# Optimization experiments

Measured on AMD Instinct MI355X. Metric: run time of the kernel, lower is better.

## Reference

```python
import jax, jax.numpy as jnp
import numpy as np

N_NODES = 50000
N_EDGES = 600000
D_IN = 128
D = 128
N_REL = 2
N_LAYERS = 3


def rgcn_conv(h, src, dst, edge_type, weight, root, bias):
    # PyG RGCNConv (no bases), aggr='mean' per relation:
    # out_i = h_i @ root + bias + sum_r mean_{j in N_r(i)} h_j @ W_r
    out = h @ root + bias                      # [N, D]
    hs = h[src]                                # [E, D] gather once
    for r in range(N_REL):
        mask = (edge_type == r).astype(h.dtype)          # [E]
        agg = jax.ops.segment_sum(hs * mask[:, None], dst, num_segments=N_NODES)  # [N, D]
        cnt = jax.ops.segment_sum(mask, dst, num_segments=N_NODES)                # [N]
        mean = agg / jnp.maximum(cnt, 1.0)[:, None]
        out = out + mean @ weight[r]
    return out


def setup_inputs() -> dict:
    key = jax.random.key(0)
    ks = jax.random.split(key, 10)
    x = jax.random.normal(ks[0], (N_NODES, D_IN), dtype=jnp.float32)
    edge_index = jax.random.randint(ks[1], (2, N_EDGES), 0, N_NODES, dtype=jnp.int64)
    edge_attr = jax.random.normal(ks[2], (N_EDGES, N_REL), dtype=jnp.float32)
    # input projection f: Linear(D_IN, D); stored as [D_IN, D] (apply as x @ Wf + bf)
    Wf = jax.random.normal(ks[3], (D_IN, D), dtype=jnp.float32) / np.sqrt(D_IN)
    bf = jnp.zeros((D,), dtype=jnp.float32)
    # per-layer RGCNConv params, stacked over layers
    conv_weight = jax.random.normal(ks[4], (N_LAYERS, N_REL, D, D), dtype=jnp.float32) / np.sqrt(D)
    conv_root = jax.random.normal(ks[5], (N_LAYERS, D, D), dtype=jnp.float32) / np.sqrt(D)
    conv_bias = jnp.zeros((N_LAYERS, D), dtype=jnp.float32)
    return {"x": x, "edge_index": edge_index, "edge_attr": edge_attr,
            "Wf": Wf, "bf": bf, "conv_weight": conv_weight,
            "conv_root": conv_root, "conv_bias": conv_bias}


def reference(x, edge_index, edge_attr, Wf, bf, conv_weight, conv_root, conv_bias):
    src, dst = edge_index[0], edge_index[1]
    edge_type = jnp.argmax(edge_attr, axis=1)           # [E]
    h = jax.nn.relu(x @ Wf + bf)                        # [N, D]
    for l in range(N_LAYERS):
        h = rgcn_conv(h, src, dst, edge_type, conv_weight[l], conv_root[l], conv_bias[l])
        h = jax.nn.relu(h)
    return h
```

## Files before the change

### kernel.cpp

```cpp
#include <hip/hip_runtime.h>
#include <hip/hip_bf16.h>

#define NN 50000
#define NE 600000
#define D 128
#define NREL 2
#define BM 128

typedef __attribute__((ext_vector_type(8))) short bf16x8;
typedef __attribute__((ext_vector_type(4))) float f32x4;
typedef __attribute__((ext_vector_type(2))) float f32x2;

__device__ __forceinline__ float bf2f(short s) {
    return __uint_as_float(((unsigned int)(unsigned short)s) << 16);
}
__device__ __forceinline__ bf16x8 pack_bf8(const float* a) {
    union { bf16x8 v; __hip_bfloat162 h2[4]; } o;
#pragma unroll
    for (int i = 0; i < 4; i++)
        o.h2[i] = __float22bfloat162_rn(make_float2(a[2 * i], a[2 * i + 1]));
    return o.v;
}

#define NEB ((NE + 255) / 256)
#define NWT (16384 + 3 * 49152)
#define NWB ((NWT + 255) / 256)

__global__ void k_pre1(const float* __restrict__ attr,
                       const int* __restrict__ dst,
                       int* __restrict__ cnt,
                       const float* __restrict__ Wf,
                       const float* __restrict__ cw,
                       const float* __restrict__ cr,
                       __hip_bfloat16* __restrict__ wt) {
    if (blockIdx.x < NEB) {
        int i = blockIdx.x * blockDim.x + threadIdx.x;
        if (i >= NE) return;
        float2 a = reinterpret_cast<const float2*>(attr)[i];
        int r = (a.y > a.x) ? 1 : 0;
        atomicAdd(&cnt[dst[i] * 2 + r], 1);
    } else {
        int idx = (blockIdx.x - NEB) * blockDim.x + threadIdx.x;
        if (idx >= NWT) return;
        float v;
        if (idx < 16384) {
            int n = idx >> 7, k = idx & 127;
            v = Wf[k * 128 + n];
        } else {
            int j = idx - 16384;
            int l = j / 49152; j %= 49152;
            int n = j / 384, k = j % 384;
            if (k < 128)      v = cr[((size_t)l * 128 + k) * 128 + n];
            else if (k < 256) v = cw[((size_t)(l * 2 + 0) * 128 + (k - 128)) * 128 + n];
            else              v = cw[((size_t)(l * 2 + 1) * 128 + (k - 256)) * 128 + n];
        }
        wt[idx] = __float2bfloat16(v);
    }
}

__global__ void k_pre2(const int* __restrict__ cnt, float* __restrict__ inv,
                       int* __restrict__ off, int* __restrict__ cur,
                       int* __restrict__ total) {
    int i = blockIdx.x * blockDim.x + threadIdx.x;
    if (i >= NN) return;
    int c0 = cnt[2 * i], c1 = cnt[2 * i + 1];
    inv[2 * i]     = 1.0f / (float)(c0 > 1 ? c0 : 1);
    inv[2 * i + 1] = 1.0f / (float)(c1 > 1 ? c1 : 1);
    int o = atomicAdd(total, c0 + c1);
    off[2 * i] = o;       cur[2 * i] = o;
    off[2 * i + 1] = o + c0; cur[2 * i + 1] = o + c0;
}

__global__ void k_fill(const float* __restrict__ attr,
                       const int* __restrict__ src, const int* __restrict__ dst,
                       int* __restrict__ cursor, int* __restrict__ srcs, int E) {
    int i = blockIdx.x * blockDim.x + threadIdx.x;
    if (i >= E) return;
    float2 a = reinterpret_cast<const float2*>(attr)[i];
    int r = (a.y > a.x) ? 1 : 0;
    int pos = atomicAdd(&cursor[dst[i] * 2 + r], 1);
    srcs[pos] = src[i];
}

__global__ __launch_bounds__(256)
void k_aggregate(const __hip_bfloat16* __restrict__ h,
                 const int* __restrict__ srcs,
                 const int* __restrict__ off, const int* __restrict__ cnt,
                 const float* __restrict__ inv,
                 __hip_bfloat16* __restrict__ agg) {
    int wid = (blockIdx.x * blockDim.x + threadIdx.x) >> 6;
    int lane = threadIdx.x & 63;
    int nb = wid * 4;
    if (nb >= NN) return;
    const int g = lane >> 4, l16 = lane & 15;
    int node = nb + g;
    bool nv = node < NN;
    int nn = nv ? node : (NN - 1);

    int st  = off[2 * nn];
    int c0  = nv ? cnt[2 * nn] : 0;
    int c01 = c0 + (nv ? cnt[2 * nn + 1] : 0);
    float i0 = inv[2 * nn], i1 = inv[2 * nn + 1];

    int sv = (l16 < c01) ? srcs[st + l16] : 0;

    int cm = c01;
    cm = max(cm, __shfl_xor(cm, 16));
    cm = max(cm, __shfl_xor(cm, 32));

    f32x2 a0[4], a1[4];
#pragma unroll
    for (int p = 0; p < 4; p++) { a0[p] = (f32x2)(0.f); a1[p] = (f32x2)(0.f); }

    const char* hb = (const char*)h;
    for (int j = 0; j < cm; j += 4) {
        int s[4]; float w0[4], w1[4];
#pragma unroll
        for (int q = 0; q < 4; ++q) {
            int jj = j + q;
            int t = __shfl(sv, (lane & 48) + (jj & 15));
            s[q] = t;
            if (jj >= 16 && jj < c01) s[q] = srcs[st + jj];
            if (jj >= c01) s[q] = 0;
            w0[q] = (jj < c0) ? i0 : 0.f;
            w1[q] = (jj >= c0 && jj < c01) ? i1 : 0.f;
        }
        uint4 v[4];
#pragma unroll
        for (int q = 0; q < 4; ++q)
            v[q] = *reinterpret_cast<const uint4*>(
                hb + (size_t)s[q] * 256 + l16 * 16);
#pragma unroll
        for (int q = 0; q < 4; ++q) {
            f32x2 w0v = {w0[q], w0[q]}, w1v = {w1[q], w1[q]};
            unsigned uu[4] = {v[q].x, v[q].y, v[q].z, v[q].w};
#pragma unroll
            for (int p = 0; p < 4; ++p) {
                f32x2 val;
                val.x = __uint_as_float(uu[p] << 16);
                val.y = __uint_as_float(uu[p] & 0xffff0000u);
                a0[p] += val * w0v;
                a1[p] += val * w1v;
            }
        }
    }

    if (!nv) return;
    float t0[8], t1[8];
#pragma unroll
    for (int p = 0; p < 4; p++) {
        t0[2 * p] = a0[p].x; t0[2 * p + 1] = a0[p].y;
        t1[2 * p] = a1[p].x; t1[2 * p + 1] = a1[p].y;
    }
    __hip_bfloat16* dp = agg + (size_t)node * 256;
    *reinterpret_cast<bf16x8*>(dp + l16 * 8)       = pack_bf8(t0);
    *reinterpret_cast<bf16x8*>(dp + 128 + l16 * 8) = pack_bf8(t1);
}

__global__ __launch_bounds__(256)
void k_gemm_proj(const float* __restrict__ X,
                 const __hip_bfloat16* __restrict__ Wt,
                 const float* __restrict__ bias,
                 __hip_bfloat16* __restrict__ out, int N) {
    __shared__ uint4 sB4[1024];
    char* sB = (char*)sB4;
    const int tid = threadIdx.x;
    const int w = tid >> 6;
    const int l16 = tid & 15, lg = (tid & 63) >> 4;

    f32x4 acc[2][8];
#pragma unroll
    for (int m = 0; m < 2; m++)
#pragma unroll
        for (int n = 0; n < 8; n++) acc[m][n] = (f32x4)(0.f);

    const int row0 = blockIdx.x * 128;
#pragma unroll
    for (int kb = 0; kb < 2; ++kb) {
        bf16x8 afr[2][2];
#pragma unroll
        for (int mb = 0; mb < 2; ++mb)
#pragma unroll
            for (int kk = 0; kk < 2; ++kk) {
                int r = row0 + w * 32 + mb * 16 + l16;
                if (r >= N) r = N - 1;
                const float* p = X + (size_t)r * D + kb * 64 + kk * 32 + lg * 8;
                float4 u0 = reinterpret_cast<const float4*>(p)[0];
                float4 u1 = reinterpret_cast<const float4*>(p)[1];
                float t[8] = {u0.x, u0.y, u0.z, u0.w, u1.x, u1.y, u1.z, u1.w};
                afr[mb][kk] = pack_bf8(t);
            }
        __syncthreads();
        {
            int trow = tid >> 3, tb = (tid & 7) * 16;
#pragma unroll
            for (int p = 0; p < 4; ++p) {
                int rr = trow + p * 32;
                uint4 v = *reinterpret_cast<const uint4*>(
                    (const char*)(Wt + (size_t)rr * 128 + kb * 64) + tb);
                *reinterpret_cast<uint4*>(sB + rr * 128 + (tb ^ ((rr & 7) << 4))) = v;
            }
        }
        __syncthreads();
#pragma unroll
        for (int kk = 0; kk < 2; ++kk)
#pragma unroll
            for (int nb = 0; nb < 8; ++nb) {
                int brow = nb * 16 + l16;
                int bcol = kk * 64 + lg * 16;
                bf16x8 bfr = *reinterpret_cast<const bf16x8*>(
                    sB + brow * 128 + (bcol ^ ((brow & 7) << 4)));
                acc[0][nb] = __builtin_amdgcn_mfma_f32_16x16x32_bf16(
                    afr[0][kk], bfr, acc[0][nb], 0, 0, 0);
                acc[1][nb] = __builtin_amdgcn_mfma_f32_16x16x32_bf16(
                    afr[1][kk], bfr, acc[1][nb], 0, 0, 0);
            }
    }
#pragma unroll
    for (int nb = 0; nb < 8; ++nb) {
        int n = nb * 16 + l16;
        float bv = bias[n];
#pragma unroll
        for (int mb = 0; mb < 2; ++mb)
#pragma unroll
            for (int r = 0; r < 4; ++r) {
                int grow = row0 + w * 32 + mb * 16 + lg * 4 + r;
                if (grow < N) {
                    float v = acc[mb][nb][r] + bv;
                    v = v > 0.f ? v : 0.f;
                    out[(size_t)grow * D + n] = __float2bfloat16(v);
                }
            }
    }
}

template <bool OUT_F32>
__global__ __launch_bounds__(256)
void k_gemm_mfma(const __hip_bfloat16* __restrict__ A0, int sA0,
                 const __hip_bfloat16* __restrict__ A1, int sA1,
                 const __hip_bfloat16* __restrict__ A2, int sA2,
                 const __hip_bfloat16* __restrict__ Wt,
                 const float* __restrict__ bias,
                 void* __restrict__ outv, int N) {
    __shared__ uint4 sB4[1024];
    char* sB = (char*)sB4;
    const int tid = threadIdx.x;
    const int w = tid >> 6;
    const int l16 = tid & 15, lg = (tid & 63) >> 4;
    const __hip_bfloat16* As[3] = {A0, A1, A2};
    const int strides[3] = {sA0, sA1, sA2};

    f32x4 acc[2][8];
#pragma unroll
    for (int m = 0; m < 2; m++)
#pragma unroll
        for (int n = 0; n < 8; n++) acc[m][n] = (f32x4)(0.f);

    const size_t row0 = (size_t)blockIdx.x * BM;
#pragma unroll
    for (int kb = 0; kb < 6; ++kb) {
        const __hip_bfloat16* Ac = As[kb >> 1];
        const int strideC = strides[kb >> 1];
        const int koff = (kb & 1) * 64;
        bf16x8 afr[2][2];
#pragma unroll
        for (int mb = 0; mb < 2; ++mb)
#pragma unroll
            for (int kk = 0; kk < 2; ++kk) {
                int r = (int)row0 + w * 32 + mb * 16 + l16;
                if (r >= N) r = N - 1;
                afr[mb][kk] = *reinterpret_cast<const bf16x8*>(
                    Ac + (size_t)r * strideC + koff + kk * 32 + lg * 8);
            }
        __syncthreads();
        {
            int trow = tid >> 3;
            int tb = (tid & 7) * 16;
#pragma unroll
            for (int p = 0; p < 4; ++p) {
                int rr = trow + p * 32;
                uint4 v = *reinterpret_cast<const uint4*>(
                    (const char*)(Wt + (size_t)rr * 384 + kb * 64) + tb);
                *reinterpret_cast<uint4*>(sB + rr * 128 + (tb ^ ((rr & 7) << 4))) = v;
            }
        }
        __syncthreads();
#pragma unroll
        for (int kk = 0; kk < 2; ++kk) {
#pragma unroll
            for (int nb = 0; nb < 8; ++nb) {
                int brow = nb * 16 + l16;
                int bcol = kk * 64 + lg * 16;
                bf16x8 bfr = *reinterpret_cast<const bf16x8*>(
                    sB + brow * 128 + (bcol ^ ((brow & 7) << 4)));
                acc[0][nb] = __builtin_amdgcn_mfma_f32_16x16x32_bf16(
                    afr[0][kk], bfr, acc[0][nb], 0, 0, 0);
                acc[1][nb] = __builtin_amdgcn_mfma_f32_16x16x32_bf16(
                    afr[1][kk], bfr, acc[1][nb], 0, 0, 0);
            }
        }
    }
#pragma unroll
    for (int nb = 0; nb < 8; ++nb) {
        int n = nb * 16 + l16;
        float bv = bias[n];
#pragma unroll
        for (int mb = 0; mb < 2; ++mb) {
#pragma unroll
            for (int r = 0; r < 4; ++r) {
                long grow = (long)row0 + w * 32 + mb * 16 + lg * 4 + r;
                if (grow < N) {
                    float v = acc[mb][nb][r] + bv;
                    v = v > 0.f ? v : 0.f;
                    if (OUT_F32)
                        ((float*)outv)[(size_t)grow * D + n] = v;
                    else
                        ((__hip_bfloat16*)outv)[(size_t)grow * D + n] =
                            __float2bfloat16(v);
                }
            }
        }
    }
}

extern "C" void kernel_launch(void* const* d_in, const int* in_sizes, int n_in,
                              void* d_out, int out_size, void* d_ws, size_t ws_size,
                              hipStream_t stream) {
    const float* x    = (const float*)d_in[0];
    const int*   ei   = (const int*)d_in[1];
    const float* attr = (const float*)d_in[2];
    const float* Wf   = (const float*)d_in[3];
    const float* bf   = (const float*)d_in[4];
    const float* cw   = (const float*)d_in[5];
    const float* cr   = (const float*)d_in[6];
    const float* cb   = (const float*)d_in[7];
    const int* src  = ei;
    const int* dstv = ei + NE;

    char* p = (char*)d_ws;
    __hip_bfloat16* h0   = (__hip_bfloat16*)p; p += (size_t)NN * D * 2;
    __hip_bfloat16* h1   = (__hip_bfloat16*)p; p += (size_t)NN * D * 2;
    __hip_bfloat16* aggb = (__hip_bfloat16*)p; p += (size_t)2 * NN * D * 2;
    __hip_bfloat16* wt   = (__hip_bfloat16*)p; p += (size_t)NWT * 2;
    float* inv  = (float*)p;                p += (size_t)2 * NN * 4;
    int*   cnt  = (int*)p;                  p += (size_t)2 * NN * 4;
    int*   off  = (int*)p;                  p += (size_t)2 * NN * 4;
    int*   cur  = (int*)p;                  p += (size_t)2 * NN * 4;
    int*   srcs = (int*)p;                  p += (size_t)NE * 4;
    int*   total= (int*)p;

    float* outp = (float*)d_out;

    hipMemsetAsync(cnt, 0, (size_t)2 * NN * sizeof(int), stream);
    hipMemsetAsync(total, 0, sizeof(int), stream);
    k_pre1<<<NEB + NWB, 256, 0, stream>>>(attr, dstv, cnt, Wf, cw, cr, wt);
    k_pre2<<<(NN + 255) / 256, 256, 0, stream>>>(cnt, inv, off, cur, total);
    k_fill<<<NEB, 256, 0, stream>>>(attr, src, dstv, cur, srcs, NE);

    k_gemm_proj<<<(NN + 127) / 128, 256, 0, stream>>>(x, wt, bf, h0, NN);

    const int gblocks = (NN + BM - 1) / BM;
    const int ablocks = ((NN + 3) / 4 * 64 + 255) / 256;
    for (int l = 0; l < 3; ++l) {
        const __hip_bfloat16* hin = (l == 1) ? h1 : h0;
        k_aggregate<<<ablocks, 256, 0, stream>>>(hin, srcs, off, cnt, inv, aggb);
        const __hip_bfloat16* wl = wt + 16384 + (size_t)l * 49152;
        const float* bl = cb + (size_t)l * D;
        if (l == 2) {
            k_gemm_mfma<true><<<gblocks, 256, 0, stream>>>(
                hin, 128, aggb, 256, aggb + 128, 256, wl, bl, outp, NN);
        } else {
            __hip_bfloat16* hout = (l == 0) ? h1 : h0;
            k_gemm_mfma<false><<<gblocks, 256, 0, stream>>>(
                hin, 128, aggb, 256, aggb + 128, 256, wl, bl, hout, NN);
        }
    }
}
```

Baseline: 230.2 us.

## Sort nodes by degree so aggregate wavefronts process similar-degree nodes

Adds a degree histogram, a single-block scan and a scatter pass that build a permutation of nodes ordered by descending total in-degree. The aggregate kernel then gives each wavefront four nodes of similar degree, which cuts divergence from the per-wave max-degree loop bound. It also adds a fast path for waves whose max degree fits in the 16 preloaded source indices. The cost is three extra small preprocessing launches with atomics, and output rows are now written in scattered rather than sequential order.

```diff
diff --git a/kernel.cpp b/kernel.cpp
--- a/kernel.cpp
+++ b/kernel.cpp
@@ -6,6 +6,7 @@
 #define D 128
 #define NREL 2
 #define BM 128
+#define NBIN 512
 
 typedef __attribute__((ext_vector_type(8))) short bf16x8;
 typedef __attribute__((ext_vector_type(4))) float f32x4;
@@ -60,7 +61,7 @@
 
 __global__ void k_pre2(const int* __restrict__ cnt, float* __restrict__ inv,
                        int* __restrict__ off, int* __restrict__ cur,
-                       int* __restrict__ total) {
+                       int* __restrict__ total, int* __restrict__ hist) {
     int i = blockIdx.x * blockDim.x + threadIdx.x;
     if (i >= NN) return;
     int c0 = cnt[2 * i], c1 = cnt[2 * i + 1];
@@ -69,6 +70,33 @@
     int o = atomicAdd(total, c0 + c1);
     off[2 * i] = o;       cur[2 * i] = o;
     off[2 * i + 1] = o + c0; cur[2 * i + 1] = o + c0;
+    int b = c0 + c1; if (b > NBIN - 1) b = NBIN - 1;
+    atomicAdd(&hist[b], 1);
+}
+
+__global__ __launch_bounds__(NBIN)
+void k_pre3(const int* __restrict__ hist, int* __restrict__ cursor) {
+    __shared__ int s[NBIN];
+    int t = threadIdx.x;
+    s[t] = hist[NBIN - 1 - t];
+    __syncthreads();
+    for (int d = 1; d < NBIN; d <<= 1) {
+        int v = (t >= d) ? s[t - d] : 0;
+        __syncthreads();
+        s[t] += v;
+        __syncthreads();
+    }
+    cursor[t] = s[NBIN - 1 - t] - hist[t];
+}
+
+__global__ void k_pre4(const int* __restrict__ cnt, int* __restrict__ cursor,
+                       int* __restrict__ order) {
+    int i = blockIdx.x * blockDim.x + threadIdx.x;
+    if (i >= NN) return;
+    int b = cnt[2 * i] + cnt[2 * i + 1];
+    if (b > NBIN - 1) b = NBIN - 1;
+    int pos = atomicAdd(&cursor[b], 1);
+    order[pos] = i;
 }
 
 __global__ void k_fill(const float* __restrict__ attr,
@@ -87,20 +115,19 @@
                  const int* __restrict__ srcs,
                  const int* __restrict__ off, const int* __restrict__ cnt,
                  const float* __restrict__ inv,
+                 const int* __restrict__ order,
                  __hip_bfloat16* __restrict__ agg) {
     int wid = (blockIdx.x * blockDim.x + threadIdx.x) >> 6;
     int lane = threadIdx.x & 63;
     int nb = wid * 4;
     if (nb >= NN) return;
     const int g = lane >> 4, l16 = lane & 15;
-    int node = nb + g;
-    bool nv = node < NN;
-    int nn = nv ? node : (NN - 1);
-
-    int st  = off[2 * nn];
-    int c0  = nv ? cnt[2 * nn] : 0;
-    int c01 = c0 + (nv ? cnt[2 * nn + 1] : 0);
-    float i0 = inv[2 * nn], i1 = inv[2 * nn + 1];
+    int node = order[nb + g];
+
+    int st  = off[2 * node];
+    int c0  = cnt[2 * node];
+    int c01 = c0 + cnt[2 * node + 1];
+    float i0 = inv[2 * node], i1 = inv[2 * node + 1];
 
     int sv = (l16 < c01) ? srcs[st + l16] : 0;
 
@@ -113,39 +140,70 @@
     for (int p = 0; p < 4; p++) { a0[p] = (f32x2)(0.f); a1[p] = (f32x2)(0.f); }
 
     const char* hb = (const char*)h;
-    for (int j = 0; j < cm; j += 4) {
-        int s[4]; float w0[4], w1[4];
-#pragma unroll
-        for (int q = 0; q < 4; ++q) {
-            int jj = j + q;
-            int t = __shfl(sv, (lane & 48) + (jj & 15));
-            s[q] = t;
-            if (jj >= 16 && jj < c01) s[q] = srcs[st + jj];
-            if (jj >= c01) s[q] = 0;
-            w0[q] = (jj < c0) ? i0 : 0.f;
-            w1[q] = (jj >= c0 && jj < c01) ? i1 : 0.f;
-        }
-        uint4 v[4];
-#pragma unroll
-        for (int q = 0; q < 4; ++q)
-            v[q] = *reinterpret_cast<const uint4*>(
-                hb + (size_t)s[q] * 256 + l16 * 16);
-#pragma unroll
-        for (int q = 0; q < 4; ++q) {
-            f32x2 w0v = {w0[q], w0[q]}, w1v = {w1[q], w1[q]};
-            unsigned uu[4] = {v[q].x, v[q].y, v[q].z, v[q].w};
-#pragma unroll
-            for (int p = 0; p < 4; ++p) {
-                f32x2 val;
-                val.x = __uint_as_float(uu[p] << 16);
-                val.y = __uint_as_float(uu[p] & 0xffff0000u);
-                a0[p] += val * w0v;
-                a1[p] += val * w1v;
-            }
-        }
-    }
-
-    if (!nv) return;
+    if (cm <= 16) {
+        for (int j = 0; j < cm; j += 4) {
+            int s[4]; float w0[4], w1[4];
+#pragma unroll
+            for (int q = 0; q < 4; ++q) {
+                int jj = j + q;
+                int t = __shfl(sv, (lane & 48) + (jj & 15));
+                s[q] = (jj < c01) ? t : 0;
+                w0[q] = (jj < c0) ? i0 : 0.f;
+                w1[q] = (jj >= c0 && jj < c01) ? i1 : 0.f;
+            }
+            uint4 v[4];
+#pragma unroll
+            for (int q = 0; q < 4; ++q)
+                v[q] = *reinterpret_cast<const uint4*>(
+                    hb + (size_t)s[q] * 256 + l16 * 16);
+#pragma unroll
+            for (int q = 0; q < 4; ++q) {
+                f32x2 w0v = {w0[q], w0[q]}, w1v = {w1[q], w1[q]};
+                unsigned uu[4] = {v[q].x, v[q].y, v[q].z, v[q].w};
+#pragma unroll
+                for (int p = 0; p < 4; ++p) {
+                    f32x2 val;
+                    val.x = __uint_as_float(uu[p] << 16);
+                    val.y = __uint_as_float(uu[p] & 0xffff0000u);
+                    a0[p] += val * w0v;
+                    a1[p] += val * w1v;
+                }
+            }
+        }
+    } else {
+        for (int j = 0; j < cm; j += 4) {
+            int s[4]; float w0[4], w1[4];
+#pragma unroll
+            for (int q = 0; q < 4; ++q) {
+                int jj = j + q;
+                int t = __shfl(sv, (lane & 48) + (jj & 15));
+                s[q] = t;
+                if (jj >= 16 && jj < c01) s[q] = srcs[st + jj];
+                if (jj >= c01) s[q] = 0;
+                w0[q] = (jj < c0) ? i0 : 0.f;
+                w1[q] = (jj >= c0 && jj < c01) ? i1 : 0.f;
+            }
+            uint4 v[4];
+#pragma unroll
+            for (int q = 0; q < 4; ++q)
+                v[q] = *reinterpret_cast<const uint4*>(
+                    hb + (size_t)s[q] * 256 + l16 * 16);
+#pragma unroll
+            for (int q = 0; q < 4; ++q) {
+                f32x2 w0v = {w0[q], w0[q]}, w1v = {w1[q], w1[q]};
+                unsigned uu[4] = {v[q].x, v[q].y, v[q].z, v[q].w};
+#pragma unroll
+                for (int p = 0; p < 4; ++p) {
+                    f32x2 val;
+                    val.x = __uint_as_float(uu[p] << 16);
+                    val.y = __uint_as_float(uu[p] & 0xffff0000u);
+                    a0[p] += val * w0v;
+                    a1[p] += val * w1v;
+                }
+            }
+        }
+    }
+
     float t0[8], t1[8];
 #pragma unroll
     for (int p = 0; p < 4; p++) {
@@ -344,17 +402,21 @@
     __hip_bfloat16* wt   = (__hip_bfloat16*)p; p += (size_t)NWT * 2;
     float* inv  = (float*)p;                p += (size_t)2 * NN * 4;
     int*   cnt  = (int*)p;                  p += (size_t)2 * NN * 4;
+    int*   hist = (int*)p;                  p += (size_t)NBIN * 4;
+    int*   total= (int*)p;                  p += 4;
     int*   off  = (int*)p;                  p += (size_t)2 * NN * 4;
     int*   cur  = (int*)p;                  p += (size_t)2 * NN * 4;
-    int*   srcs = (int*)p;                  p += (size_t)NE * 4;
-    int*   total= (int*)p;
+    int*   bcur = (int*)p;                  p += (size_t)NBIN * 4;
+    int*   order= (int*)p;                  p += (size_t)NN * 4;
+    int*   srcs = (int*)p;
 
     float* outp = (float*)d_out;
 
-    hipMemsetAsync(cnt, 0, (size_t)2 * NN * sizeof(int), stream);
-    hipMemsetAsync(total, 0, sizeof(int), stream);
+    hipMemsetAsync(cnt, 0, (size_t)(2 * NN + NBIN + 1) * sizeof(int), stream);
     k_pre1<<<NEB + NWB, 256, 0, stream>>>(attr, dstv, cnt, Wf, cw, cr, wt);
-    k_pre2<<<(NN + 255) / 256, 256, 0, stream>>>(cnt, inv, off, cur, total);
+    k_pre2<<<(NN + 255) / 256, 256, 0, stream>>>(cnt, inv, off, cur, total, hist);
+    k_pre3<<<1, NBIN, 0, stream>>>(hist, bcur);
+    k_pre4<<<(NN + 255) / 256, 256, 0, stream>>>(cnt, bcur, order);
     k_fill<<<NEB, 256, 0, stream>>>(attr, src, dstv, cur, srcs, NE);
 
     k_gemm_proj<<<(NN + 127) / 128, 256, 0, stream>>>(x, wt, bf, h0, NN);
@@ -363,7 +425,8 @@
     const int ablocks = ((NN + 3) / 4 * 64 + 255) / 256;
     for (int l = 0; l < 3; ++l) {
         const __hip_bfloat16* hin = (l == 1) ? h1 : h0;
-        k_aggregate<<<ablocks, 256, 0, stream>>>(hin, srcs, off, cnt, inv, aggb);
+        k_aggregate<<<ablocks, 256, 0, stream>>>(hin, srcs, off, cnt, inv,
+                                                 order, aggb);
         const __hip_bfloat16* wl = wt + 16384 + (size_t)l * 49152;
         const float* bl = cb + (size_t)l * D;
         if (l == 2) {
```

Measured after the change: 534.4 us. 2.32x slower.
